# Optimization experiments

Hardware: AMD Instinct MI355X
Metric: run time of the kernel (lower is better)

## Reference

```python
import math
import jax, jax.numpy as jnp
import numpy as np

N_FEAT = 4096
EPS = 1e-05
SQRT_LUT = jnp.array([math.isqrt(i * 256 + 128) for i in range(256)], dtype=jnp.int32)


def _ste_round(x):
    # straight-through round: forward round, backward identity
    return x + jax.lax.stop_gradient(jnp.round(x) - x)


def _sqrt_rounded(d):
    # vectorized integer LUT sqrt of d (int32, values in [0, 65535])
    bits = jnp.arange(16, dtype=jnp.int32)
    msb = jnp.sum((d[..., None] >> bits) > 0, axis=-1).astype(jnp.int32) - 1  # bit_length - 1
    k = msb // 2
    norm_shift = (7 - k) * 2
    d_norm = d << norm_shift
    lut_addr = (d_norm >> 8) & 255
    mant = SQRT_LUT[lut_addr]
    q_floor = mant >> (7 - k)
    boundary = q_floor * q_floor + q_floor
    res = jnp.where(d > boundary, q_floor + 1, q_floor)
    return jnp.where(d == 0, 0, res)


def setup_inputs() -> dict:
    key = jax.random.key(0)
    kx, = jax.random.split(key, 1)
    x = jax.random.normal(kx, (8192, N_FEAT), dtype=jnp.float32)
    gamma = jnp.ones((N_FEAT,), dtype=jnp.float32)
    beta = jnp.zeros((N_FEAT,), dtype=jnp.float32)
    return {"x": x, "gamma": gamma, "beta": beta}


def reference(x, gamma, beta):
    # input quantization (per-tensor symmetric int8)
    scale_in = jnp.maximum(jnp.max(jnp.abs(x)) / 127.0, 1e-08)
    x_int = jnp.clip(_ste_round(x / scale_in), -127.0, 127.0)
    x_q = x_int * scale_in
    Ex = jnp.sum(x_q, axis=1, keepdims=True)  # [B,1]
    # LUT-based squaring: split |x_int| into high/low nibbles, x^2 = H^2*256 + 2*H*L*16 + L^2
    X_abs = jnp.abs(x_int).astype(jnp.int32)  # int cast detaches (matches .long())
    H = X_abs >> 4
    L = X_abs & 15
    x_squared_int = (H * H * 256 + H * L * 32 + L * L).astype(jnp.float32)
    x_squared_q = x_squared_int * scale_in ** 2
    Ex2 = jnp.sum(x_squared_q, axis=1, keepdims=True)  # [B,1]
    mu = Ex / N_FEAT
    var = jnp.maximum(Ex2 / N_FEAT - mu * mu, 0.0)
    var_int = jnp.clip(jnp.round(var), 1.0, 2.0 ** 16 - 1).astype(jnp.int32)
    std_int = _sqrt_rounded(var_int).astype(jnp.float32)  # [B,1]
    inv_std = 1.0 / jnp.maximum(std_int, EPS)
    x_norm = (x_q - mu) * inv_std
    y = x_norm * gamma + beta
    # output re-quantization
    scale_out = jnp.maximum(jnp.max(jnp.abs(y)) / 127.0, 1e-08)
    y_int = jnp.clip(_ste_round(y / scale_out), -127.0, 127.0)
    return y_int * scale_out
```

## Files before the change

### kernel.cpp

```cpp
#include <hip/hip_runtime.h>
#include <hip/hip_cooperative_groups.h>
#include <stdint.h>

namespace cg = cooperative_groups;

#define NFEAT 4096
#define UI_PER_ROW (NFEAT / 4)
#define GRID 256
#define BLK 1024
#define ROWS_PB 32

#define NSLOT 64
#define SLOT_STRIDE 16

__device__ __forceinline__ int isqrt_floor_small(int v) {
    int m = (int)sqrtf((float)v);
    m -= (m * m > v);
    m += ((m + 1) * (m + 1) <= v);
    return m;
}

__device__ __forceinline__ int sqrt_rounded_ref(int d) {
    if (d <= 0) return 0;
    int msb = 31 - __clz(d);
    int k = msb >> 1;
    int sh = (7 - k) * 2;
    int dn = d << sh;
    int la = (dn >> 8) & 255;
    int mant = isqrt_floor_small(la * 256 + 128);
    int qf = mant >> (7 - k);
    int bnd = qf * qf + qf;
    return (d > bnd) ? (qf + 1) : qf;
}

__device__ __forceinline__ float div_rn(float x, float s, float rs) {
    float q0 = x * rs;
    float r  = fmaf(-s, q0, x);
    return fmaf(r, rs, q0);
}

__device__ __forceinline__ float slots256_max(const unsigned* __restrict__ s, int lane) {
    unsigned v = s[lane];
    unsigned a = s[lane + 64], b = s[lane + 128], c = s[lane + 192];
    v = v > a ? v : a;
    v = v > b ? v : b;
    v = v > c ? v : c;
#pragma unroll
    for (int off = 32; off; off >>= 1) {
        unsigned o = (unsigned)__shfl_xor((int)v, off);
        v = v > o ? v : o;
    }
    return __uint_as_float(v);
}

__global__ __launch_bounds__(BLK, 4) void fused_kernel(
    const float* __restrict__ x, const float* __restrict__ gamma,
    const float* __restrict__ beta, float* __restrict__ out,
    unsigned* __restrict__ slot, unsigned* __restrict__ slot2, int rows) {
#pragma clang fp contract(off)
    cg::grid_group gridg = cg::this_grid();
    const int bid = blockIdx.x;
    const int t = threadIdx.x;
    const int lane = t & 63;
    const int wave = t >> 6;

    __shared__ int a1s[16], a2s[16];
    __shared__ float redf[16];
    __shared__ float smu[ROWS_PB], sinv[ROWS_PB];

    {
        const float4* x4 = (const float4*)x;
        const int n4 = rows * (NFEAT / 4);
        const int stride = GRID * BLK;
        int i = bid * BLK + t;
        float m = 0.0f;
        for (; i + 3 * stride < n4; i += 4 * stride) {
            float4 a = x4[i];
            float4 b = x4[i + stride];
            float4 c = x4[i + 2 * stride];
            float4 d = x4[i + 3 * stride];
            float ma = fmaxf(fmaxf(fabsf(a.x), fabsf(a.y)), fmaxf(fabsf(a.z), fabsf(a.w)));
            float mb = fmaxf(fmaxf(fabsf(b.x), fabsf(b.y)), fmaxf(fabsf(b.z), fabsf(b.w)));
            float mc = fmaxf(fmaxf(fabsf(c.x), fabsf(c.y)), fmaxf(fabsf(c.z), fabsf(c.w)));
            float md = fmaxf(fmaxf(fabsf(d.x), fabsf(d.y)), fmaxf(fabsf(d.z), fabsf(d.w)));
            m = fmaxf(m, fmaxf(fmaxf(ma, mb), fmaxf(mc, md)));
        }
        for (; i < n4; i += stride) {
            float4 a = x4[i];
            m = fmaxf(m, fmaxf(fmaxf(fabsf(a.x), fabsf(a.y)), fmaxf(fabsf(a.z), fabsf(a.w))));
        }
#pragma unroll
        for (int off = 32; off; off >>= 1) m = fmaxf(m, __shfl_down(m, off));
        if (lane == 0) redf[wave] = m;
        __syncthreads();
        if (t == 0) {
            float mm = redf[0];
#pragma unroll
            for (int i2 = 1; i2 < 16; ++i2) mm = fmaxf(mm, redf[i2]);
            slot[bid] = __float_as_uint(mm);
        }
    }
    gridg.sync();

    const float s  = fmaxf(slots256_max(slot, lane) / 127.0f, 1e-8f);
    const float rs = 1.0f / s;
    const int rb = t >> 8;
    const int tr = t & 255;
    const int nb = ROWS_PB / 4;
    float ym = 0.0f;
    for (int b = 0; b < nb; ++b) {
        const int r = bid * ROWS_PB + b * 4 + rb;
        const float4* xr = (const float4*)(x + (size_t)r * NFEAT);
        float4 v0 = xr[tr];
        float4 v1 = xr[256 + tr];
        float4 v2 = xr[512 + tr];
        float4 v3 = xr[768 + tr];
        float xv[16] = {v0.x, v0.y, v0.z, v0.w, v1.x, v1.y, v1.z, v1.w,
                        v2.x, v2.y, v2.z, v2.w, v3.x, v3.y, v3.z, v3.w};
        int xi[16];
        int s1 = 0, s2 = 0;
#pragma unroll
        for (int k = 0; k < 16; ++k) {
            float q = rintf(div_rn(xv[k], s, rs));
            q = fminf(fmaxf(q, -127.0f), 127.0f);
            int qi = (int)q;
            xi[k] = qi;
            s1 += qi;
            s2 += qi * qi;
        }
#pragma unroll
        for (int off = 32; off; off >>= 1) {
            s1 += __shfl_down(s1, off);
            s2 += __shfl_down(s2, off);
        }
        if (lane == 0) { a1s[wave] = s1; a2s[wave] = s2; }
        __syncthreads();
        if (tr == 0) {
            const int w0 = rb * 4;
            int Exi  = a1s[w0] + a1s[w0 + 1] + a1s[w0 + 2] + a1s[w0 + 3];
            int Ex2i = a2s[w0] + a2s[w0 + 1] + a2s[w0 + 2] + a2s[w0 + 3];
            float Ex  = (float)Exi * s;
            float Ex2 = (float)Ex2i * s * s;
            float mu  = Ex / (float)NFEAT;
            float var = fmaxf(Ex2 / (float)NFEAT - mu * mu, 0.0f);
            float vr  = fminf(fmaxf(rintf(var), 1.0f), 65535.0f);
            int std_int = sqrt_rounded_ref((int)vr);
            float inv = 1.0f / fmaxf((float)std_int, 1e-5f);
            smu[b * 4 + rb]  = mu;
            sinv[b * 4 + rb] = inv;
        }
        __syncthreads();
        const float mu = smu[b * 4 + rb], inv = sinv[b * 4 + rb];
#pragma unroll
        for (int g = 0; g < 4; ++g) {
            float4 gm = ((const float4*)gamma)[g * 256 + tr];
            float4 bt = ((const float4*)beta)[g * 256 + tr];
            float gv[4] = {gm.x, gm.y, gm.z, gm.w};
            float bv[4] = {bt.x, bt.y, bt.z, bt.w};
#pragma unroll
            for (int j = 0; j < 4; ++j) {
                float xq = (float)xi[g * 4 + j] * s;
                float xn = (xq - mu) * inv;
                float y = xn * gv[j] + bv[j];
                ym = fmaxf(ym, fabsf(y));
            }
        }
    }
#pragma unroll
    for (int off = 32; off; off >>= 1) ym = fmaxf(ym, __shfl_down(ym, off));
    if (lane == 0) redf[wave] = ym;
    __syncthreads();
    if (t == 0) {
        float mm = redf[0];
#pragma unroll
        for (int i2 = 1; i2 < 16; ++i2) mm = fmaxf(mm, redf[i2]);
        slot2[bid] = __float_as_uint(mm);
    }
    gridg.sync();

    const float so  = fmaxf(slots256_max(slot2, lane) / 127.0f, 1e-8f);
    const float rso = 1.0f / so;
    for (int b = 0; b < nb; ++b) {
        const int r = bid * ROWS_PB + b * 4 + rb;
        const float4* xr = (const float4*)(x + (size_t)r * NFEAT);
        float4 v0 = xr[tr];
        float4 v1 = xr[256 + tr];
        float4 v2 = xr[512 + tr];
        float4 v3 = xr[768 + tr];
        float xv[16] = {v0.x, v0.y, v0.z, v0.w, v1.x, v1.y, v1.z, v1.w,
                        v2.x, v2.y, v2.z, v2.w, v3.x, v3.y, v3.z, v3.w};
        const float mu = smu[b * 4 + rb], inv = sinv[b * 4 + rb];
        float4* outr = (float4*)(out + (size_t)r * NFEAT);
#pragma unroll
        for (int g = 0; g < 4; ++g) {
            float4 gm = ((const float4*)gamma)[g * 256 + tr];
            float4 bt = ((const float4*)beta)[g * 256 + tr];
            float gv[4] = {gm.x, gm.y, gm.z, gm.w};
            float bv[4] = {bt.x, bt.y, bt.z, bt.w};
            float o[4];
#pragma unroll
            for (int j = 0; j < 4; ++j) {
                float q = rintf(div_rn(xv[g * 4 + j], s, rs));
                q = fminf(fmaxf(q, -127.0f), 127.0f);
                float xq = q * s;
                float xn = (xq - mu) * inv;
                float y = xn * gv[j] + bv[j];
                float qq = rintf(div_rn(y, so, rso));
                qq = fminf(fmaxf(qq, -127.0f), 127.0f);
                o[j] = qq * so;
            }
            outr[g * 256 + tr] = make_float4(o[0], o[1], o[2], o[3]);
        }
    }
}

__device__ __forceinline__ float slot_max64(const unsigned* __restrict__ slots) {
    unsigned v = slots[(threadIdx.x & 63) * SLOT_STRIDE];
#pragma unroll
    for (int off = 32; off; off >>= 1) {
        unsigned o = (unsigned)__shfl_xor((int)v, off);
        v = v > o ? v : o;
    }
    return __uint_as_float(v);
}

__global__ __launch_bounds__(256, 4) void absmax_kernel(const float* __restrict__ x,
                                                        int n4,
                                                        unsigned* __restrict__ hx) {
    const float4* x4 = (const float4*)x;
    int i = blockIdx.x * 256 + threadIdx.x;
    const int stride = gridDim.x * 256;
    float m = 0.0f;
    for (; i + 3 * stride < n4; i += 4 * stride) {
        float4 a = x4[i];
        float4 b = x4[i + stride];
        float4 c = x4[i + 2 * stride];
        float4 d = x4[i + 3 * stride];
        float ma = fmaxf(fmaxf(fabsf(a.x), fabsf(a.y)), fmaxf(fabsf(a.z), fabsf(a.w)));
        float mb = fmaxf(fmaxf(fabsf(b.x), fabsf(b.y)), fmaxf(fabsf(b.z), fabsf(b.w)));
        float mc = fmaxf(fmaxf(fabsf(c.x), fabsf(c.y)), fmaxf(fabsf(c.z), fabsf(c.w)));
        float md = fmaxf(fmaxf(fabsf(d.x), fabsf(d.y)), fmaxf(fabsf(d.z), fabsf(d.w)));
        m = fmaxf(m, fmaxf(fmaxf(ma, mb), fmaxf(mc, md)));
    }
    for (; i < n4; i += stride) {
        float4 a = x4[i];
        m = fmaxf(m, fmaxf(fmaxf(fabsf(a.x), fabsf(a.y)), fmaxf(fabsf(a.z), fabsf(a.w))));
    }
#pragma unroll
    for (int off = 32; off; off >>= 1) m = fmaxf(m, __shfl_down(m, off));
    __shared__ float smax[4];
    int lane = threadIdx.x & 63, w = threadIdx.x >> 6;
    if (lane == 0) smax[w] = m;
    __syncthreads();
    if (threadIdx.x == 0) {
        m = fmaxf(fmaxf(smax[0], smax[1]), fmaxf(smax[2], smax[3]));
        atomicMax(hx + (blockIdx.x & (NSLOT - 1)) * SLOT_STRIDE, __float_as_uint(m));
    }
}

__global__ __launch_bounds__(256, 4) void rowstat_kernel(
    const float* __restrict__ x, const float* __restrict__ gamma,
    const float* __restrict__ beta, const unsigned* __restrict__ hx,
    unsigned* __restrict__ hy,
    float* __restrict__ row_mu, float* __restrict__ row_inv) {
#pragma clang fp contract(off)
    const int row = blockIdx.x;
    const int t = threadIdx.x;
    const float4* xr = (const float4*)(x + (size_t)row * NFEAT);
    float4 v0 = xr[t];
    float4 v1 = xr[256 + t];
    float4 v2 = xr[512 + t];
    float4 v3 = xr[768 + t];
    const float s  = fmaxf(slot_max64(hx) / 127.0f, 1e-8f);
    const float rs = 1.0f / s;

    float xv[16] = {v0.x, v0.y, v0.z, v0.w, v1.x, v1.y, v1.z, v1.w,
                    v2.x, v2.y, v2.z, v2.w, v3.x, v3.y, v3.z, v3.w};
    int xi[16];
    int s1 = 0, s2 = 0;
#pragma unroll
    for (int k = 0; k < 16; ++k) {
        float q = rintf(div_rn(xv[k], s, rs));
        q = fminf(fmaxf(q, -127.0f), 127.0f);
        int qi = (int)q;
        xi[k] = qi;
        s1 += qi;
        s2 += qi * qi;
    }
#pragma unroll
    for (int off = 32; off; off >>= 1) {
        s1 += __shfl_down(s1, off);
        s2 += __shfl_down(s2, off);
    }
    __shared__ int a1[4], a2[4];
    __shared__ float smu1, sinv1;
    const int lane = t & 63, w = t >> 6;
    if (lane == 0) { a1[w] = s1; a2[w] = s2; }
    __syncthreads();
    if (t == 0) {
        int Exi = a1[0] + a1[1] + a1[2] + a1[3];
        int Ex2i = a2[0] + a2[1] + a2[2] + a2[3];
        float Ex = (float)Exi * s;
        float Ex2 = (float)Ex2i * s * s;
        float mu = Ex / (float)NFEAT;
        float var = fmaxf(Ex2 / (float)NFEAT - mu * mu, 0.0f);
        float vr = fminf(fmaxf(rintf(var), 1.0f), 65535.0f);
        int std_int = sqrt_rounded_ref((int)vr);
        float inv_std = 1.0f / fmaxf((float)std_int, 1e-5f);
        row_mu[row] = mu;
        row_inv[row] = inv_std;
        smu1 = mu;
        sinv1 = inv_std;
    }
    __syncthreads();
    const float mu = smu1, inv = sinv1;
    float ym = 0.0f;
#pragma unroll
    for (int g = 0; g < 4; ++g) {
        float4 gm = ((const float4*)gamma)[g * 256 + t];
        float4 bt = ((const float4*)beta)[g * 256 + t];
        float gv[4] = {gm.x, gm.y, gm.z, gm.w};
        float bv[4] = {bt.x, bt.y, bt.z, bt.w};
#pragma unroll
        for (int j = 0; j < 4; ++j) {
            float xq = (float)xi[g * 4 + j] * s;
            float xn = (xq - mu) * inv;
            float y = xn * gv[j] + bv[j];
            ym = fmaxf(ym, fabsf(y));
        }
    }
#pragma unroll
    for (int off = 32; off; off >>= 1) ym = fmaxf(ym, __shfl_down(ym, off));
    __shared__ float aym[4];
    if (lane == 0) aym[w] = ym;
    __syncthreads();
    if (t == 0) {
        float m = fmaxf(fmaxf(aym[0], aym[1]), fmaxf(aym[2], aym[3]));
        atomicMax(hy + (row & (NSLOT - 1)) * SLOT_STRIDE, __float_as_uint(m));
    }
}

__global__ __launch_bounds__(256, 4) void quantout_f_kernel(
    const float* __restrict__ x, const float* __restrict__ gamma,
    const float* __restrict__ beta, const unsigned* __restrict__ hx,
    const unsigned* __restrict__ hy,
    const float* __restrict__ row_mu, const float* __restrict__ row_inv,
    float* __restrict__ out) {
#pragma clang fp contract(off)
    const int row = blockIdx.x;
    const int t = threadIdx.x;
    const float4* xr = (const float4*)(x + (size_t)row * NFEAT);
    float4 w0 = xr[t];
    float4 w1 = xr[256 + t];
    float4 w2 = xr[512 + t];
    float4 w3 = xr[768 + t];
    const float s_in  = fmaxf(slot_max64(hx) / 127.0f, 1e-8f);
    const float s_out = fmaxf(slot_max64(hy) / 127.0f, 1e-8f);
    const float rsi = 1.0f / s_in;
    const float rso = 1.0f / s_out;
    const float mu = row_mu[row], inv = row_inv[row];
    float4 vv[4] = {w0, w1, w2, w3};
    float4* outr = (float4*)(out + (size_t)row * NFEAT);
#pragma unroll
    for (int g = 0; g < 4; ++g) {
        float4 v = vv[g];
        float4 gm = ((const float4*)gamma)[g * 256 + t];
        float4 bt = ((const float4*)beta)[g * 256 + t];
        float xv[4] = {v.x, v.y, v.z, v.w};
        float gv[4] = {gm.x, gm.y, gm.z, gm.w};
        float bv[4] = {bt.x, bt.y, bt.z, bt.w};
        float o[4];
#pragma unroll
        for (int j = 0; j < 4; ++j) {
            float q = rintf(div_rn(xv[j], s_in, rsi));
            q = fminf(fmaxf(q, -127.0f), 127.0f);
            float xq = q * s_in;
            float xn = (xq - mu) * inv;
            float y = xn * gv[j] + bv[j];
            float qq = rintf(div_rn(y, s_out, rso));
            qq = fminf(fmaxf(qq, -127.0f), 127.0f);
            o[j] = qq * s_out;
        }
        outr[g * 256 + t] = make_float4(o[0], o[1], o[2], o[3]);
    }
}

extern "C" void kernel_launch(void* const* d_in, const int* in_sizes, int n_in,
                              void* d_out, int out_size, void* d_ws, size_t ws_size,
                              hipStream_t stream) {
    const float* x = (const float*)d_in[0];
    const float* gamma = (const float*)d_in[1];
    const float* beta = (const float*)d_in[2];
    float* out = (float*)d_out;

    const int total = in_sizes[0];
    int rows = total / NFEAT;

    char* ws = (char*)d_ws;
    unsigned* slot  = (unsigned*)ws;
    unsigned* slot2 = (unsigned*)(ws + 2048);

    if (rows == GRID * ROWS_PB) {
        void* args[] = {(void*)&x, (void*)&gamma, (void*)&beta, (void*)&out,
                        (void*)&slot, (void*)&slot2, (void*)&rows};
        hipError_t e = hipLaunchCooperativeKernel((void*)fused_kernel,
                                                  dim3(GRID), dim3(BLK),
                                                  args, 0, stream);
        if (e == hipSuccess) return;
    }

    unsigned* hx = (unsigned*)ws;
    unsigned* hy = (unsigned*)(ws + 4096);
    float* row_mu = (float*)(ws + 8192);
    float* row_inv = row_mu + rows;

    hipMemsetAsync(ws, 0, 8192, stream);
    absmax_kernel<<<2048, 256, 0, stream>>>(x, total / 4, hx);
    rowstat_kernel<<<rows, 256, 0, stream>>>(x, gamma, beta, hx, hy,
                                             row_mu, row_inv);
    quantout_f_kernel<<<rows, 256, 0, stream>>>(x, gamma, beta, hx, hy,
                                                row_mu, row_inv, out);
}
```

Before: 342.5 us.

## Keep quantized rows packed in registers and map one wave per row

The cooperative kernel now launches 512 blocks of 512 threads. Each wave owns two full rows, so the per-row statistics reduce with wave shuffles only and the block-level shared-memory syncs go away. The int8-quantized values are packed four per register and kept across both grid syncs, so the final phase no longer re-reads x from global memory and re-quantizes it. The cost is higher register pressure from 32 packed words per thread, plus a larger cooperative grid that must still fit co-resident on the device.

```diff
diff --git a/kernel.cpp b/kernel.cpp
--- a/kernel.cpp
+++ b/kernel.cpp
@@ -5,10 +5,9 @@
 namespace cg = cooperative_groups;
 
 #define NFEAT 4096
-#define UI_PER_ROW (NFEAT / 4)
-#define GRID 256
-#define BLK 1024
-#define ROWS_PB 32
+#define GRID 512
+#define BLK 512
+#define ROWS_PB 16
 
 #define NSLOT 64
 #define SLOT_STRIDE 16
@@ -39,12 +38,13 @@
     return fmaf(r, rs, q0);
 }
 
-__device__ __forceinline__ float slots256_max(const unsigned* __restrict__ s, int lane) {
-    unsigned v = s[lane];
-    unsigned a = s[lane + 64], b = s[lane + 128], c = s[lane + 192];
-    v = v > a ? v : a;
-    v = v > b ? v : b;
-    v = v > c ? v : c;
+__device__ __forceinline__ float slots_max(const unsigned* __restrict__ s, int lane) {
+    unsigned v = 0;
+#pragma unroll
+    for (int i = 0; i < GRID / 64; ++i) {
+        unsigned a = s[lane + i * 64];
+        v = v > a ? v : a;
+    }
 #pragma unroll
     for (int off = 32; off; off >>= 1) {
         unsigned o = (unsigned)__shfl_xor((int)v, off);
@@ -52,6 +52,90 @@
     }
     return __uint_as_float(v);
 }
+
+#define P2_ROW(PK, MU, INV, ROWIDX)                                           \
+    {                                                                         \
+        const float4* xr4 = (const float4*)(x + (size_t)(ROWIDX) * NFEAT);    \
+        int s1 = 0, s2 = 0;                                                   \
+        _Pragma("unroll")                                                     \
+        for (int c = 0; c < 16; ++c) {                                        \
+            float4 v = xr4[c * 64 + lane];                                    \
+            float q0 = rintf(div_rn(v.x, s, rs));                             \
+            float q1 = rintf(div_rn(v.y, s, rs));                             \
+            float q2 = rintf(div_rn(v.z, s, rs));                             \
+            float q3 = rintf(div_rn(v.w, s, rs));                             \
+            q0 = fminf(fmaxf(q0, -127.0f), 127.0f);                           \
+            q1 = fminf(fmaxf(q1, -127.0f), 127.0f);                           \
+            q2 = fminf(fmaxf(q2, -127.0f), 127.0f);                           \
+            q3 = fminf(fmaxf(q3, -127.0f), 127.0f);                           \
+            int i0 = (int)q0, i1 = (int)q1, i2 = (int)q2, i3 = (int)q3;       \
+            PK[c] = (uint32_t)(i0 & 255) | ((uint32_t)(i1 & 255) << 8) |      \
+                    ((uint32_t)(i2 & 255) << 16) | ((uint32_t)i3 << 24);      \
+            s1 += i0 + i1 + i2 + i3;                                          \
+            s2 += i0 * i0 + i1 * i1 + i2 * i2 + i3 * i3;                      \
+        }                                                                     \
+        _Pragma("unroll")                                                     \
+        for (int off = 32; off; off >>= 1) {                                  \
+            s1 += __shfl_xor(s1, off);                                        \
+            s2 += __shfl_xor(s2, off);                                        \
+        }                                                                     \
+        float Ex  = (float)s1 * s;                                            \
+        float Ex2 = (float)s2 * s * s;                                        \
+        float mu_ = Ex / (float)NFEAT;                                        \
+        float var = fmaxf(Ex2 / (float)NFEAT - mu_ * mu_, 0.0f);              \
+        float vr  = fminf(fmaxf(rintf(var), 1.0f), 65535.0f);                 \
+        int sdi   = sqrt_rounded_ref((int)vr);                                \
+        MU  = mu_;                                                            \
+        INV = 1.0f / fmaxf((float)sdi, 1e-5f);                                \
+    }
+
+#define P2_YMAX(PK, MU, INV, YM)                                              \
+    {                                                                         \
+        _Pragma("unroll")                                                     \
+        for (int c = 0; c < 16; ++c) {                                        \
+            uint32_t p = PK[c];                                               \
+            float4 gm = g4[c * 64 + lane];                                    \
+            float4 bt = b4[c * 64 + lane];                                    \
+            int i0 = (int)(int8_t)(p & 255);                                  \
+            int i1 = (int)(int8_t)((p >> 8) & 255);                           \
+            int i2 = (int)(int8_t)((p >> 16) & 255);                          \
+            int i3 = (int)(int8_t)((p >> 24) & 255);                          \
+            float y0 = ((float)i0 * s - (MU)) * (INV) * gm.x + bt.x;          \
+            float y1 = ((float)i1 * s - (MU)) * (INV) * gm.y + bt.y;          \
+            float y2 = ((float)i2 * s - (MU)) * (INV) * gm.z + bt.z;          \
+            float y3 = ((float)i3 * s - (MU)) * (INV) * gm.w + bt.w;          \
+            YM = fmaxf(YM, fmaxf(fmaxf(fabsf(y0), fabsf(y1)),                 \
+                                 fmaxf(fabsf(y2), fabsf(y3))));               \
+        }                                                                     \
+    }
+
+#define P3_ROW(PK, MU, INV, ROWIDX)                                           \
+    {                                                                         \
+        float4* o4 = (float4*)(out + (size_t)(ROWIDX) * NFEAT);               \
+        _Pragma("unroll")                                                     \
+        for (int c = 0; c < 16; ++c) {                                        \
+            uint32_t p = PK[c];                                               \
+            float4 gm = g4[c * 64 + lane];                                    \
+            float4 bt = b4[c * 64 + lane];                                    \
+            int i0 = (int)(int8_t)(p & 255);                                  \
+            int i1 = (int)(int8_t)((p >> 8) & 255);                           \
+            int i2 = (int)(int8_t)((p >> 16) & 255);                          \
+            int i3 = (int)(int8_t)((p >> 24) & 255);                          \
+            float y0 = ((float)i0 * s - (MU)) * (INV) * gm.x + bt.x;          \
+            float y1 = ((float)i1 * s - (MU)) * (INV) * gm.y + bt.y;          \
+            float y2 = ((float)i2 * s - (MU)) * (INV) * gm.z + bt.z;          \
+            float y3 = ((float)i3 * s - (MU)) * (INV) * gm.w + bt.w;          \
+            float q0 = rintf(div_rn(y0, so, rso));                            \
+            float q1 = rintf(div_rn(y1, so, rso));                            \
+            float q2 = rintf(div_rn(y2, so, rso));                            \
+            float q3 = rintf(div_rn(y3, so, rso));                            \
+            q0 = fminf(fmaxf(q0, -127.0f), 127.0f);                           \
+            q1 = fminf(fmaxf(q1, -127.0f), 127.0f);                           \
+            q2 = fminf(fmaxf(q2, -127.0f), 127.0f);                           \
+            q3 = fminf(fmaxf(q3, -127.0f), 127.0f);                           \
+            o4[c * 64 + lane] = make_float4(q0 * so, q1 * so, q2 * so, q3 * so); \
+        }                                                                     \
+    }
 
 __global__ __launch_bounds__(BLK, 4) void fused_kernel(
     const float* __restrict__ x, const float* __restrict__ gamma,
@@ -63,10 +147,10 @@
     const int t = threadIdx.x;
     const int lane = t & 63;
     const int wave = t >> 6;
-
-    __shared__ int a1s[16], a2s[16];
-    __shared__ float redf[16];
-    __shared__ float smu[ROWS_PB], sinv[ROWS_PB];
+    const float4* g4 = (const float4*)gamma;
+    const float4* b4 = (const float4*)beta;
+
+    __shared__ float redf[BLK / 64];
 
     {
         const float4* x4 = (const float4*)x;
@@ -96,76 +180,27 @@
         if (t == 0) {
             float mm = redf[0];
 #pragma unroll
-            for (int i2 = 1; i2 < 16; ++i2) mm = fmaxf(mm, redf[i2]);
+            for (int i2 = 1; i2 < BLK / 64; ++i2) mm = fmaxf(mm, redf[i2]);
             slot[bid] = __float_as_uint(mm);
         }
+        __syncthreads();
     }
     gridg.sync();
 
-    const float s  = fmaxf(slots256_max(slot, lane) / 127.0f, 1e-8f);
+    const float s  = fmaxf(slots_max(slot, lane) / 127.0f, 1e-8f);
     const float rs = 1.0f / s;
-    const int rb = t >> 8;
-    const int tr = t & 255;
-    const int nb = ROWS_PB / 4;
+    const int gw = bid * (BLK / 64) + wave;
+    const int r0 = gw * 2;
+    const int r1 = gw * 2 + 1;
+
+    uint32_t pkA[16], pkB[16];
+    float muA, invA, muB, invB;
+    P2_ROW(pkA, muA, invA, r0)
+    P2_ROW(pkB, muB, invB, r1)
+
     float ym = 0.0f;
-    for (int b = 0; b < nb; ++b) {
-        const int r = bid * ROWS_PB + b * 4 + rb;
-        const float4* xr = (const float4*)(x + (size_t)r * NFEAT);
-        float4 v0 = xr[tr];
-        float4 v1 = xr[256 + tr];
-        float4 v2 = xr[512 + tr];
-        float4 v3 = xr[768 + tr];
-        float xv[16] = {v0.x, v0.y, v0.z, v0.w, v1.x, v1.y, v1.z, v1.w,
-                        v2.x, v2.y, v2.z, v2.w, v3.x, v3.y, v3.z, v3.w};
-        int xi[16];
-        int s1 = 0, s2 = 0;
-#pragma unroll
-        for (int k = 0; k < 16; ++k) {
-            float q = rintf(div_rn(xv[k], s, rs));
-            q = fminf(fmaxf(q, -127.0f), 127.0f);
-            int qi = (int)q;
-            xi[k] = qi;
-            s1 += qi;
-            s2 += qi * qi;
-        }
-#pragma unroll
-        for (int off = 32; off; off >>= 1) {
-            s1 += __shfl_down(s1, off);
-            s2 += __shfl_down(s2, off);
-        }
-        if (lane == 0) { a1s[wave] = s1; a2s[wave] = s2; }
-        __syncthreads();
-        if (tr == 0) {
-            const int w0 = rb * 4;
-            int Exi  = a1s[w0] + a1s[w0 + 1] + a1s[w0 + 2] + a1s[w0 + 3];
-            int Ex2i = a2s[w0] + a2s[w0 + 1] + a2s[w0 + 2] + a2s[w0 + 3];
-            float Ex  = (float)Exi * s;
-            float Ex2 = (float)Ex2i * s * s;
-            float mu  = Ex / (float)NFEAT;
-            float var = fmaxf(Ex2 / (float)NFEAT - mu * mu, 0.0f);
-            float vr  = fminf(fmaxf(rintf(var), 1.0f), 65535.0f);
-            int std_int = sqrt_rounded_ref((int)vr);
-            float inv = 1.0f / fmaxf((float)std_int, 1e-5f);
-            smu[b * 4 + rb]  = mu;
-            sinv[b * 4 + rb] = inv;
-        }
-        __syncthreads();
-        const float mu = smu[b * 4 + rb], inv = sinv[b * 4 + rb];
-#pragma unroll
-        for (int g = 0; g < 4; ++g) {
-            float4 gm = ((const float4*)gamma)[g * 256 + tr];
-            float4 bt = ((const float4*)beta)[g * 256 + tr];
-            float gv[4] = {gm.x, gm.y, gm.z, gm.w};
-            float bv[4] = {bt.x, bt.y, bt.z, bt.w};
-#pragma unroll
-            for (int j = 0; j < 4; ++j) {
-                float xq = (float)xi[g * 4 + j] * s;
-                float xn = (xq - mu) * inv;
-                float y = xn * gv[j] + bv[j];
-                ym = fmaxf(ym, fabsf(y));
-            }
-        }
-    }
+    P2_YMAX(pkA, muA, invA, ym)
+    P2_YMAX(pkB, muB, invB, ym)
 #pragma unroll
     for (int off = 32; off; off >>= 1) ym = fmaxf(ym, __shfl_down(ym, off));
     if (lane == 0) redf[wave] = ym;
@@ -173,45 +208,15 @@
     if (t == 0) {
         float mm = redf[0];
 #pragma unroll
-        for (int i2 = 1; i2 < 16; ++i2) mm = fmaxf(mm, redf[i2]);
+        for (int i2 = 1; i2 < BLK / 64; ++i2) mm = fmaxf(mm, redf[i2]);
         slot2[bid] = __float_as_uint(mm);
     }
     gridg.sync();
 
-    const float so  = fmaxf(slots256_max(slot2, lane) / 127.0f, 1e-8f);
+    const float so  = fmaxf(slots_max(slot2, lane) / 127.0f, 1e-8f);
     const float rso = 1.0f / so;
-    for (int b = 0; b < nb; ++b) {
-        const int r = bid * ROWS_PB + b * 4 + rb;
-        const float4* xr = (const float4*)(x + (size_t)r * NFEAT);
-        float4 v0 = xr[tr];
-        float4 v1 = xr[256 + tr];
-        float4 v2 = xr[512 + tr];
-        float4 v3 = xr[768 + tr];
-        float xv[16] = {v0.x, v0.y, v0.z, v0.w, v1.x, v1.y, v1.z, v1.w,
-                        v2.x, v2.y, v2.z, v2.w, v3.x, v3.y, v3.z, v3.w};
-        const float mu = smu[b * 4 + rb], inv = sinv[b * 4 + rb];
-        float4* outr = (float4*)(out + (size_t)r * NFEAT);
-#pragma unroll
-        for (int g = 0; g < 4; ++g) {
-            float4 gm = ((const float4*)gamma)[g * 256 + tr];
-            float4 bt = ((const float4*)beta)[g * 256 + tr];
-            float gv[4] = {gm.x, gm.y, gm.z, gm.w};
-            float bv[4] = {bt.x, bt.y, bt.z, bt.w};
-            float o[4];
-#pragma unroll
-            for (int j = 0; j < 4; ++j) {
-                float q = rintf(div_rn(xv[g * 4 + j], s, rs));
-                q = fminf(fmaxf(q, -127.0f), 127.0f);
-                float xq = q * s;
-                float xn = (xq - mu) * inv;
-                float y = xn * gv[j] + bv[j];
-                float qq = rintf(div_rn(y, so, rso));
-                qq = fminf(fmaxf(qq, -127.0f), 127.0f);
-                o[j] = qq * so;
-            }
-            outr[g * 256 + tr] = make_float4(o[0], o[1], o[2], o[3]);
-        }
-    }
+    P3_ROW(pkA, muA, invA, r0)
+    P3_ROW(pkB, muB, invB, r1)
 }
 
 __device__ __forceinline__ float slot_max64(const unsigned* __restrict__ slots) {
@@ -398,7 +403,7 @@
 
     char* ws = (char*)d_ws;
     unsigned* slot  = (unsigned*)ws;
-    unsigned* slot2 = (unsigned*)(ws + 2048);
+    unsigned* slot2 = (unsigned*)(ws + 4096);
 
     if (rows == GRID * ROWS_PB) {
         void* args[] = {(void*)&x, (void*)&gamma, (void*)&beta, (void*)&out,
```

After: 606.4 us. 77.1% more time.

## Restructure cooperative kernel to wave-per-row ownership with grid of 1024x256

Applied to the files above, without the earlier changes.

The cooperative fused kernel now uses 1024 blocks of 256 threads, and each wave owns two full rows. Row statistics are reduced with wave shuffles only, which drops the per-row __syncthreads and shared-memory reductions. Phase 1 reads exactly the rows the wave later processes, which may improve cache locality for the re-reads in phases 2 and 3. Quantized values are kept packed as int8 in registers between the stats and absmax passes. The risks are higher register pressure, since 16 packed words per row are held for two rows, and that the 1024-block cooperative launch must fit co-resident at 4 blocks per CU.

```diff
diff --git a/kernel.cpp b/kernel.cpp
--- a/kernel.cpp
+++ b/kernel.cpp
@@ -5,10 +5,10 @@
 namespace cg = cooperative_groups;
 
 #define NFEAT 4096
-#define UI_PER_ROW (NFEAT / 4)
-#define GRID 256
-#define BLK 1024
-#define ROWS_PB 32
+#define GRID 1024
+#define BLK 256
+#define WPB (BLK / 64)
+#define RPW 2
 
 #define NSLOT 64
 #define SLOT_STRIDE 16
@@ -39,18 +39,106 @@
     return fmaf(r, rs, q0);
 }
 
-__device__ __forceinline__ float slots256_max(const unsigned* __restrict__ s, int lane) {
-    unsigned v = s[lane];
-    unsigned a = s[lane + 64], b = s[lane + 128], c = s[lane + 192];
-    v = v > a ? v : a;
-    v = v > b ? v : b;
-    v = v > c ? v : c;
+__device__ __forceinline__ float slots_max(const unsigned* __restrict__ s, int lane) {
+    unsigned v = 0;
+#pragma unroll
+    for (int i = 0; i < GRID / 64; ++i) {
+        unsigned a = s[lane + i * 64];
+        v = v > a ? v : a;
+    }
 #pragma unroll
     for (int off = 32; off; off >>= 1) {
         unsigned o = (unsigned)__shfl_xor((int)v, off);
         v = v > o ? v : o;
     }
     return __uint_as_float(v);
+}
+
+__device__ __forceinline__ void p2_row(const float4* __restrict__ xr4,
+                                       const float4* __restrict__ g4,
+                                       const float4* __restrict__ b4,
+                                       int lane, float s, float rs,
+                                       float& mu_out, float& inv_out, float& ym) {
+    uint32_t pk[16];
+    int s1 = 0, s2 = 0;
+#pragma unroll
+    for (int c = 0; c < 16; ++c) {
+        float4 v = xr4[c * 64 + lane];
+        float q0 = rintf(div_rn(v.x, s, rs));
+        float q1 = rintf(div_rn(v.y, s, rs));
+        float q2 = rintf(div_rn(v.z, s, rs));
+        float q3 = rintf(div_rn(v.w, s, rs));
+        q0 = fminf(fmaxf(q0, -127.0f), 127.0f);
+        q1 = fminf(fmaxf(q1, -127.0f), 127.0f);
+        q2 = fminf(fmaxf(q2, -127.0f), 127.0f);
+        q3 = fminf(fmaxf(q3, -127.0f), 127.0f);
+        int i0 = (int)q0, i1 = (int)q1, i2 = (int)q2, i3 = (int)q3;
+        pk[c] = (uint32_t)(i0 & 255) | ((uint32_t)(i1 & 255) << 8) |
+                ((uint32_t)(i2 & 255) << 16) | ((uint32_t)i3 << 24);
+        s1 += i0 + i1 + i2 + i3;
+        s2 += i0 * i0 + i1 * i1 + i2 * i2 + i3 * i3;
+    }
+#pragma unroll
+    for (int off = 32; off; off >>= 1) {
+        s1 += __shfl_xor(s1, off);
+        s2 += __shfl_xor(s2, off);
+    }
+    float Ex  = (float)s1 * s;
+    float Ex2 = (float)s2 * s * s;
+    float mu  = Ex / (float)NFEAT;
+    float var = fmaxf(Ex2 / (float)NFEAT - mu * mu, 0.0f);
+    float vr  = fminf(fmaxf(rintf(var), 1.0f), 65535.0f);
+    int sdi   = sqrt_rounded_ref((int)vr);
+    float inv = 1.0f / fmaxf((float)sdi, 1e-5f);
+#pragma unroll
+    for (int c = 0; c < 16; ++c) {
+        uint32_t p = pk[c];
+        float4 gm = g4[c * 64 + lane];
+        float4 bt = b4[c * 64 + lane];
+        int i0 = (int)(int8_t)(p & 255);
+        int i1 = (int)(int8_t)((p >> 8) & 255);
+        int i2 = (int)(int8_t)((p >> 16) & 255);
+        int i3 = (int)(int8_t)((p >> 24) & 255);
+        float y0 = ((float)i0 * s - mu) * inv * gm.x + bt.x;
+        float y1 = ((float)i1 * s - mu) * inv * gm.y + bt.y;
+        float y2 = ((float)i2 * s - mu) * inv * gm.z + bt.z;
+        float y3 = ((float)i3 * s - mu) * inv * gm.w + bt.w;
+        ym = fmaxf(ym, fmaxf(fmaxf(fabsf(y0), fabsf(y1)),
+                             fmaxf(fabsf(y2), fabsf(y3))));
+    }
+    mu_out = mu;
+    inv_out = inv;
+}
+
+__device__ __forceinline__ void p3_row(const float4* __restrict__ xr4,
+                                       const float4* __restrict__ g4,
+                                       const float4* __restrict__ b4,
+                                       float4* __restrict__ o4,
+                                       int lane, float s, float rs,
+                                       float mu, float inv, float so, float rso) {
+#pragma unroll
+    for (int c = 0; c < 16; ++c) {
+        float4 v = xr4[c * 64 + lane];
+        float4 gm = g4[c * 64 + lane];
+        float4 bt = b4[c * 64 + lane];
+        float q0 = rintf(div_rn(v.x, s, rs));
+        float q1 = rintf(div_rn(v.y, s, rs));
+        float q2 = rintf(div_rn(v.z, s, rs));
+        float q3 = rintf(div_rn(v.w, s, rs));
+        q0 = fminf(fmaxf(q0, -127.0f), 127.0f);
+        q1 = fminf(fmaxf(q1, -127.0f), 127.0f);
+        q2 = fminf(fmaxf(q2, -127.0f), 127.0f);
+        q3 = fminf(fmaxf(q3, -127.0f), 127.0f);
+        float y0 = (q0 * s - mu) * inv * gm.x + bt.x;
+        float y1 = (q1 * s - mu) * inv * gm.y + bt.y;
+        float y2 = (q2 * s - mu) * inv * gm.z + bt.z;
+        float y3 = (q3 * s - mu) * inv * gm.w + bt.w;
+        float o0 = fminf(fmaxf(rintf(div_rn(y0, so, rso)), -127.0f), 127.0f) * so;
+        float o1 = fminf(fmaxf(rintf(div_rn(y1, so, rso)), -127.0f), 127.0f) * so;
+        float o2 = fminf(fmaxf(rintf(div_rn(y2, so, rso)), -127.0f), 127.0f) * so;
+        float o3 = fminf(fmaxf(rintf(div_rn(y3, so, rso)), -127.0f), 127.0f) * so;
+        o4[c * 64 + lane] = make_float4(o0, o1, o2, o3);
+    }
 }
 
 __global__ __launch_bounds__(BLK, 4) void fused_kernel(
@@ -63,31 +151,26 @@
     const int t = threadIdx.x;
     const int lane = t & 63;
     const int wave = t >> 6;
-
-    __shared__ int a1s[16], a2s[16];
-    __shared__ float redf[16];
-    __shared__ float smu[ROWS_PB], sinv[ROWS_PB];
+    const float4* g4 = (const float4*)gamma;
+    const float4* b4 = (const float4*)beta;
+
+    __shared__ float redf[WPB];
+
+    const int gw = bid * WPB + wave;
+    const float4* xA = (const float4*)(x + (size_t)gw * RPW * NFEAT);
+    const float4* xB = xA + NFEAT / 4;
+    float4* oA = (float4*)(out + (size_t)gw * RPW * NFEAT);
+    float4* oB = oA + NFEAT / 4;
 
     {
-        const float4* x4 = (const float4*)x;
-        const int n4 = rows * (NFEAT / 4);
-        const int stride = GRID * BLK;
-        int i = bid * BLK + t;
         float m = 0.0f;
-        for (; i + 3 * stride < n4; i += 4 * stride) {
-            float4 a = x4[i];
-            float4 b = x4[i + stride];
-            float4 c = x4[i + 2 * stride];
-            float4 d = x4[i + 3 * stride];
+#pragma unroll
+        for (int c = 0; c < 16; ++c) {
+            float4 a = xA[c * 64 + lane];
+            float4 b = xB[c * 64 + lane];
             float ma = fmaxf(fmaxf(fabsf(a.x), fabsf(a.y)), fmaxf(fabsf(a.z), fabsf(a.w)));
             float mb = fmaxf(fmaxf(fabsf(b.x), fabsf(b.y)), fmaxf(fabsf(b.z), fabsf(b.w)));
-            float mc = fmaxf(fmaxf(fabsf(c.x), fabsf(c.y)), fmaxf(fabsf(c.z), fabsf(c.w)));
-            float md = fmaxf(fmaxf(fabsf(d.x), fabsf(d.y)), fmaxf(fabsf(d.z), fabsf(d.w)));
-            m = fmaxf(m, fmaxf(fmaxf(ma, mb), fmaxf(mc, md)));
-        }
-        for (; i < n4; i += stride) {
-            float4 a = x4[i];
-            m = fmaxf(m, fmaxf(fmaxf(fabsf(a.x), fabsf(a.y)), fmaxf(fabsf(a.z), fabsf(a.w))));
+            m = fmaxf(m, fmaxf(ma, mb));
         }
 #pragma unroll
         for (int off = 32; off; off >>= 1) m = fmaxf(m, __shfl_down(m, off));
@@ -96,76 +179,19 @@
         if (t == 0) {
             float mm = redf[0];
 #pragma unroll
-            for (int i2 = 1; i2 < 16; ++i2) mm = fmaxf(mm, redf[i2]);
+            for (int i2 = 1; i2 < WPB; ++i2) mm = fmaxf(mm, redf[i2]);
             slot[bid] = __float_as_uint(mm);
         }
+        __syncthreads();
     }
     gridg.sync();
 
-    const float s  = fmaxf(slots256_max(slot, lane) / 127.0f, 1e-8f);
+    const float s  = fmaxf(slots_max(slot, lane) / 127.0f, 1e-8f);
     const float rs = 1.0f / s;
-    const int rb = t >> 8;
-    const int tr = t & 255;
-    const int nb = ROWS_PB / 4;
+    float muA, invA, muB, invB;
     float ym = 0.0f;
-    for (int b = 0; b < nb; ++b) {
-        const int r = bid * ROWS_PB + b * 4 + rb;
-        const float4* xr = (const float4*)(x + (size_t)r * NFEAT);
-        float4 v0 = xr[tr];
-        float4 v1 = xr[256 + tr];
-        float4 v2 = xr[512 + tr];
-        float4 v3 = xr[768 + tr];
-        float xv[16] = {v0.x, v0.y, v0.z, v0.w, v1.x, v1.y, v1.z, v1.w,
-                        v2.x, v2.y, v2.z, v2.w, v3.x, v3.y, v3.z, v3.w};
-        int xi[16];
-        int s1 = 0, s2 = 0;
-#pragma unroll
-        for (int k = 0; k < 16; ++k) {
-            float q = rintf(div_rn(xv[k], s, rs));
-            q = fminf(fmaxf(q, -127.0f), 127.0f);
-            int qi = (int)q;
-            xi[k] = qi;
-            s1 += qi;
-            s2 += qi * qi;
-        }
-#pragma unroll
-        for (int off = 32; off; off >>= 1) {
-            s1 += __shfl_down(s1, off);
-            s2 += __shfl_down(s2, off);
-        }
-        if (lane == 0) { a1s[wave] = s1; a2s[wave] = s2; }
-        __syncthreads();
-        if (tr == 0) {
-            const int w0 = rb * 4;
-            int Exi  = a1s[w0] + a1s[w0 + 1] + a1s[w0 + 2] + a1s[w0 + 3];
-            int Ex2i = a2s[w0] + a2s[w0 + 1] + a2s[w0 + 2] + a2s[w0 + 3];
-            float Ex  = (float)Exi * s;
-            float Ex2 = (float)Ex2i * s * s;
-            float mu  = Ex / (float)NFEAT;
-            float var = fmaxf(Ex2 / (float)NFEAT - mu * mu, 0.0f);
-            float vr  = fminf(fmaxf(rintf(var), 1.0f), 65535.0f);
-            int std_int = sqrt_rounded_ref((int)vr);
-            float inv = 1.0f / fmaxf((float)std_int, 1e-5f);
-            smu[b * 4 + rb]  = mu;
-            sinv[b * 4 + rb] = inv;
-        }
-        __syncthreads();
-        const float mu = smu[b * 4 + rb], inv = sinv[b * 4 + rb];
-#pragma unroll
-        for (int g = 0; g < 4; ++g) {
-            float4 gm = ((const float4*)gamma)[g * 256 + tr];
-            float4 bt = ((const float4*)beta)[g * 256 + tr];
-            float gv[4] = {gm.x, gm.y, gm.z, gm.w};
-            float bv[4] = {bt.x, bt.y, bt.z, bt.w};
-#pragma unroll
-            for (int j = 0; j < 4; ++j) {
-                float xq = (float)xi[g * 4 + j] * s;
-                float xn = (xq - mu) * inv;
-                float y = xn * gv[j] + bv[j];
-                ym = fmaxf(ym, fabsf(y));
-            }
-        }
-    }
+    p2_row(xA, g4, b4, lane, s, rs, muA, invA, ym);
+    p2_row(xB, g4, b4, lane, s, rs, muB, invB, ym);
 #pragma unroll
     for (int off = 32; off; off >>= 1) ym = fmaxf(ym, __shfl_down(ym, off));
     if (lane == 0) redf[wave] = ym;
@@ -173,45 +199,15 @@
     if (t == 0) {
         float mm = redf[0];
 #pragma unroll
-        for (int i2 = 1; i2 < 16; ++i2) mm = fmaxf(mm, redf[i2]);
+        for (int i2 = 1; i2 < WPB; ++i2) mm = fmaxf(mm, redf[i2]);
         slot2[bid] = __float_as_uint(mm);
     }
     gridg.sync();
 
-    const float so  = fmaxf(slots256_max(slot2, lane) / 127.0f, 1e-8f);
+    const float so  = fmaxf(slots_max(slot2, lane) / 127.0f, 1e-8f);
     const float rso = 1.0f / so;
-    for (int b = 0; b < nb; ++b) {
-        const int r = bid * ROWS_PB + b * 4 + rb;
-        const float4* xr = (const float4*)(x + (size_t)r * NFEAT);
-        float4 v0 = xr[tr];
-        float4 v1 = xr[256 + tr];
-        float4 v2 = xr[512 + tr];
-        float4 v3 = xr[768 + tr];
-        float xv[16] = {v0.x, v0.y, v0.z, v0.w, v1.x, v1.y, v1.z, v1.w,
-                        v2.x, v2.y, v2.z, v2.w, v3.x, v3.y, v3.z, v3.w};
-        const float mu = smu[b * 4 + rb], inv = sinv[b * 4 + rb];
-        float4* outr = (float4*)(out + (size_t)r * NFEAT);
-#pragma unroll
-        for (int g = 0; g < 4; ++g) {
-            float4 gm = ((const float4*)gamma)[g * 256 + tr];
-            float4 bt = ((const float4*)beta)[g * 256 + tr];
-            float gv[4] = {gm.x, gm.y, gm.z, gm.w};
-            float bv[4] = {bt.x, bt.y, bt.z, bt.w};
-            float o[4];
-#pragma unroll
-            for (int j = 0; j < 4; ++j) {
-                float q = rintf(div_rn(xv[g * 4 + j], s, rs));
-                q = fminf(fmaxf(q, -127.0f), 127.0f);
-                float xq = q * s;
-                float xn = (xq - mu) * inv;
-                float y = xn * gv[j] + bv[j];
-                float qq = rintf(div_rn(y, so, rso));
-                qq = fminf(fmaxf(qq, -127.0f), 127.0f);
-                o[j] = qq * so;
-            }
-            outr[g * 256 + tr] = make_float4(o[0], o[1], o[2], o[3]);
-        }
-    }
+    p3_row(xA, g4, b4, oA, lane, s, rs, muA, invA, so, rso);
+    p3_row(xB, g4, b4, oB, lane, s, rs, muB, invB, so, rso);
 }
 
 __device__ __forceinline__ float slot_max64(const unsigned* __restrict__ slots) {
@@ -398,9 +394,9 @@
 
     char* ws = (char*)d_ws;
     unsigned* slot  = (unsigned*)ws;
-    unsigned* slot2 = (unsigned*)(ws + 2048);
-
-    if (rows == GRID * ROWS_PB) {
+    unsigned* slot2 = (unsigned*)(ws + 4096);
+
+    if (rows == GRID * WPB * RPW) {
         void* args[] = {(void*)&x, (void*)&gamma, (void*)&beta, (void*)&out,
                         (void*)&slot, (void*)&slot2, (void*)&rows};
         hipError_t e = hipLaunchCooperativeKernel((void*)fused_kernel,
```

After: 737.1 us. 2.15x slower.
